# Kernel tuning notes

Hardware: AMD Instinct MI355X
Metric: run time of the kernel (lower is better)

## Reference

```python
import jax, jax.numpy as jnp
import numpy as np

B, S, E, H, F, V = 4, 2048, 1024, 16, 4096, 32000
D = E // H  # head_dim = 64
LN_EPS = 1e-5


def layer_norm(x, g, b):
    mu = jnp.mean(x, axis=-1, keepdims=True)
    var = jnp.mean(jnp.square(x - mu), axis=-1, keepdims=True)
    return (x - mu) * jax.lax.rsqrt(var + LN_EPS) * g + b


def setup_inputs() -> dict:
    key = jax.random.key(0)
    ks = jax.random.split(key, 12)
    s = 0.02
    return {
        "input_ids": jax.random.randint(ks[0], (B, S), 0, V),
        "attention_mask": jnp.ones((B, S), dtype=jnp.int32),
        "emb_table": jax.random.normal(ks[1], (V, E), jnp.float32) * s,
        "Wq": jax.random.normal(ks[2], (E, E), jnp.float32) * s,
        "bq": jnp.zeros((E,), jnp.float32),
        "Wk": jax.random.normal(ks[3], (E, E), jnp.float32) * s,
        "bk": jnp.zeros((E,), jnp.float32),
        "Wv": jax.random.normal(ks[4], (E, E), jnp.float32) * s,
        "bv": jnp.zeros((E,), jnp.float32),
        "Wo": jax.random.normal(ks[5], (E, E), jnp.float32) * s,
        "bo": jnp.zeros((E,), jnp.float32),
        "ln_g": jnp.ones((E,), jnp.float32),
        "ln_b": jnp.zeros((E,), jnp.float32),
        "W1": jax.random.normal(ks[6], (E, F), jnp.float32) * s,
        "b1": jnp.zeros((F,), jnp.float32),
        "W2": jax.random.normal(ks[7], (F, E), jnp.float32) * s,
        "b2": jnp.zeros((E,), jnp.float32),
        "Wp": jax.random.normal(ks[8], (E, 3), jnp.float32) * s,
        "bp": jnp.zeros((3,), jnp.float32),
    }


def reference(input_ids, attention_mask, emb_table, Wq, bq, Wk, bk, Wv, bv,
              Wo, bo, ln_g, ln_b, W1, b1, W2, b2, Wp, bp):
    b, s = input_ids.shape
    x = emb_table[input_ids]                                  # [B,S,E]
    q = (x @ Wq + bq).reshape(b, s, H, D).transpose(0, 2, 1, 3)  # [B,H,S,D]
    k = (x @ Wk + bk).reshape(b, s, H, D).transpose(0, 2, 1, 3)
    v = (x @ Wv + bv).reshape(b, s, H, D).transpose(0, 2, 1, 3)
    scores = jnp.einsum('bhqd,bhkd->bhqk', q, k) / jnp.sqrt(jnp.float32(D))
    mask = attention_mask[:, None, None, :]                   # [B,1,1,S]
    scores = jnp.where(mask == 0, -jnp.inf, scores)
    attn = jax.nn.softmax(scores, axis=-1)
    ctx = jnp.einsum('bhqk,bhkd->bhqd', attn, v)              # [B,H,S,D]
    ctx = ctx.transpose(0, 2, 1, 3).reshape(b, s, E)
    ctx = ctx @ Wo + bo
    h = layer_norm(ctx + x, ln_g, ln_b)
    ff = jax.nn.gelu(h @ W1 + b1, approximate=False) @ W2 + b2
    logits = ff @ Wp + bp                                     # [B,S,3]
    return logits.mean(axis=1)                                # [B,3]
```

## Files before the change

### kernel.cpp

```cpp
#include <hip/hip_runtime.h>
#include <hip/hip_bf16.h>
#include <math.h>

#define BB 4
#define SS 2048
#define EE 1024
#define HH 16
#define DD 64
#define FF 4096

typedef unsigned short u16;
typedef unsigned int u32;
typedef __bf16 bf16x8 __attribute__((ext_vector_type(8)));
typedef float f32x4 __attribute__((ext_vector_type(4)));

static __device__ __forceinline__ float gelu_exact(float v){
  return 0.5f * v * (1.0f + erff(v * 0.70710678118654752f));
}

static __device__ __forceinline__ u16 f2bf(float f){
  union { float f; u32 u; } x; x.f = f;
  u32 r = x.u + 0x7FFFu + ((x.u >> 16) & 1u);
  return (u16)(r >> 16);
}
static __device__ __forceinline__ u16 f2bf_hw(float f){
  union { __bf16 b; u16 u; } c; c.b = (__bf16)f; return c.u;
}
static __device__ __forceinline__ void unpack2(u32 u, float& lo, float& hi){
  union { u32 u; float f; } a, b;
  a.u = u << 16; b.u = u & 0xFFFF0000u;
  lo = a.f; hi = b.f;
}

#define GLOAD_LDS16(g, l) \
  __builtin_amdgcn_global_load_lds((const __attribute__((address_space(1))) void*)(g), \
      (__attribute__((address_space(3))) void*)(l), 16, 0, 0)

__global__ __launch_bounds__(256) void embed_kernel(const int* __restrict__ ids,
    const float* __restrict__ emb, float* __restrict__ xf, u16* __restrict__ xbf){
  int row = blockIdx.x;
  int id  = ids[row];
  float4 v = ((const float4*)(emb + (size_t)id * EE))[threadIdx.x];
  ((float4*)(xf + (size_t)row * EE))[threadIdx.x] = v;
  ushort4 u; u.x = f2bf(v.x); u.y = f2bf(v.y); u.z = f2bf(v.z); u.w = f2bf(v.w);
  ((ushort4*)(xbf + (size_t)row * EE))[threadIdx.x] = u;
}

__global__ __launch_bounds__(256) void prep_weights(const float* __restrict__ Wq,
    const float* __restrict__ Wk, const float* __restrict__ Wv,
    const float* __restrict__ Wo, const float* __restrict__ W1, u16* __restrict__ WT){
  __shared__ float tile[32][33];
  int bid = blockIdx.x;
  const float* W; u16* dst; int N, n0, k0;
  if (bid < 4096){
    W = W1; dst = WT + (size_t)4 * EE * EE; N = FF;
    n0 = (bid & 127) * 32; k0 = (bid >> 7) * 32;
  } else {
    int idx = bid - 4096;
    int which = idx >> 10, t = idx & 1023;
    W = (which == 0) ? Wq : (which == 1) ? Wk : (which == 2) ? Wv : Wo;
    dst = WT + (size_t)which * EE * EE; N = EE;
    n0 = (t & 31) * 32; k0 = (t >> 5) * 32;
  }
  int tx = threadIdx.x & 31, ty = threadIdx.x >> 5;
  #pragma unroll
  for (int i = 0; i < 4; i++)
    tile[ty + 8*i][tx] = W[(size_t)(k0 + ty + 8*i) * N + n0 + tx];
  __syncthreads();
  #pragma unroll
  for (int i = 0; i < 4; i++)
    dst[(size_t)(n0 + ty + 8*i) * EE + k0 + tx] = f2bf(tile[tx][ty + 8*i]);
}

template<int MODE>
__global__ __launch_bounds__(256) void gemm_mfma(const u16* __restrict__ A,
    const u16* __restrict__ WT, const float* __restrict__ bias,
    const float* __restrict__ biasB, const float* __restrict__ biasC,
    u16* __restrict__ C, float* __restrict__ gsum, int M, int N, int K){
  __shared__ __attribute__((aligned(16))) u16 As[128 * 32];
  __shared__ __attribute__((aligned(16))) u16 Bs[128 * 32];

  const int tid = threadIdx.x;
  const int l = tid & 63, w = tid >> 6;
  const int lm = l & 15, lq = l >> 4;
  const int wm = (w >> 1) * 64, wn = (w & 1) * 64;
  const int r0 = blockIdx.y * 128, c0 = blockIdx.x * 128;

  const int srow0 = w * 32 + (l >> 2);
  const int scol  = (l & 3) * 8;
  const u16* Ab = A  + (size_t)(r0 + srow0) * K + scol;
  const u16* Bb = WT + (size_t)(c0 + srow0) * K + scol;
  u16* AsBase0 = &As[(w * 2)     * 512];
  u16* AsBase1 = &As[(w * 2 + 1) * 512];
  u16* BsBase0 = &Bs[(w * 2)     * 512];
  u16* BsBase1 = &Bs[(w * 2 + 1) * 512];

  f32x4 acc[4][4];
  const f32x4 zero = {0.f, 0.f, 0.f, 0.f};
  #pragma unroll
  for (int mi = 0; mi < 4; mi++)
    #pragma unroll
    for (int ni = 0; ni < 4; ni++) acc[mi][ni] = zero;

  for (int k0 = 0; k0 < K; k0 += 32){
    GLOAD_LDS16(Ab + k0,                    AsBase0);
    GLOAD_LDS16(Ab + (size_t)16 * K + k0,   AsBase1);
    GLOAD_LDS16(Bb + k0,                    BsBase0);
    GLOAD_LDS16(Bb + (size_t)16 * K + k0,   BsBase1);
    __syncthreads();

    bf16x8 af[4], bf[4];
    #pragma unroll
    for (int mi = 0; mi < 4; mi++)
      af[mi] = *(const bf16x8*)&As[(wm + mi*16 + lm) * 32 + lq * 8];
    #pragma unroll
    for (int ni = 0; ni < 4; ni++)
      bf[ni] = *(const bf16x8*)&Bs[(wn + ni*16 + lm) * 32 + lq * 8];
    #pragma unroll
    for (int mi = 0; mi < 4; mi++)
      #pragma unroll
      for (int ni = 0; ni < 4; ni++)
        acc[mi][ni] = __builtin_amdgcn_mfma_f32_16x16x32_bf16(af[mi], bf[ni], acc[mi][ni], 0, 0, 0);
    __syncthreads();
  }

  if constexpr (MODE == 0){
    #pragma unroll
    for (int ni = 0; ni < 4; ni++){
      int col = c0 + wn + ni*16 + lm;
      float bcol = bias[col];
      #pragma unroll
      for (int mi = 0; mi < 4; mi++){
        #pragma unroll
        for (int r = 0; r < 4; r++){
          int row = r0 + wm + mi*16 + lq*4 + r;
          C[(size_t)row * N + col] = f2bf(acc[mi][ni][r] + bcol);
        }
      }
    }
  } else if constexpr (MODE == 2){
    #pragma unroll
    for (int ni = 0; ni < 4; ni++){
      int col3 = c0 + wn + ni*16 + lm;
      int sel  = col3 >> 10;
      int colm = col3 & 1023;
      const float* bp_ = (sel == 0) ? bias : ((sel == 1) ? biasB : biasC);
      float bcol = bp_[colm];
      u16* dst = C + (size_t)sel * ((size_t)M * N);
      #pragma unroll
      for (int mi = 0; mi < 4; mi++){
        #pragma unroll
        for (int r = 0; r < 4; r++){
          int row = r0 + wm + mi*16 + lq*4 + r;
          dst[(size_t)row * N + colm] = f2bf(acc[mi][ni][r] + bcol);
        }
      }
    }
  } else {
    const int batch = r0 >> 11;
    #pragma unroll
    for (int ni = 0; ni < 4; ni++){
      int col = c0 + wn + ni*16 + lm;
      float bcol = bias[col];
      float cs = 0.f;
      #pragma unroll
      for (int mi = 0; mi < 4; mi++)
        #pragma unroll
        for (int r = 0; r < 4; r++)
          cs += gelu_exact(acc[mi][ni][r] + bcol);
      cs += __shfl_xor(cs, 16, 64);
      cs += __shfl_xor(cs, 32, 64);
      if (lq == 0) atomicAdd(&gsum[(size_t)batch * N + col], cs);
    }
  }
}

__global__ __launch_bounds__(256, 4) void attn_mfma(const u16* __restrict__ q,
    const u16* __restrict__ k, const u16* __restrict__ v,
    const int* __restrict__ mask, u16* __restrict__ ctx){
  const int bh = blockIdx.y, b = bh >> 4, h = bh & 15;
  const int q0 = blockIdx.x * 128;
  const int tid = threadIdx.x;
  const int w = tid >> 6, l = tid & 63, lm = l & 15, lq = l >> 4;

  __shared__ __attribute__((aligned(16))) u16 smem[128 * 72];
  __shared__ __attribute__((aligned(16))) float mb[64];
  u16* Kt = smem;
  u16* Vt = smem + 64 * 72;

  bf16x8 aq[2][2];
  #pragma unroll
  for (int mg = 0; mg < 2; mg++){
    const u16* qrow = q + (size_t)(b*SS + q0 + w*32 + mg*16 + lm) * EE + h*DD + lq*8;
    aq[mg][0] = *(const bf16x8*)qrow;
    aq[mg][1] = *(const bf16x8*)(qrow + 32);
  }

  f32x4 occ[2][4];
  const f32x4 zero = {0.f,0.f,0.f,0.f};
  #pragma unroll
  for (int mg = 0; mg < 2; mg++)
    #pragma unroll
    for (int mi = 0; mi < 4; mi++) occ[mg][mi] = zero;
  float l_part[2] = {0.f, 0.f};

  const int kkey = tid >> 2, kc16 = (tid & 3) * 16;
  const u16* kbase = k + (size_t)(b*SS + kkey) * EE + h*DD + kc16;
  const int kp = tid & 31, vd0 = (tid >> 5) * 8;
  const u16* vbase0 = v + (size_t)(b*SS + 2*kp) * EE + h*DD + vd0;
  const u16* vbase1 = vbase0 + EE;

  uint4 kr0 = *(const uint4*)(kbase);
  uint4 kr1 = *(const uint4*)(kbase + 8);
  uint4 vr0 = *(const uint4*)(vbase0);
  uint4 vr1 = *(const uint4*)(vbase1);
  float mreg = 0.f;
  if (tid < 64) mreg = (mask[b*SS + tid] != 0) ? 0.f : -1e30f;

  const float SCALE_LOG2E = 0.125f * 1.4426950408889634f;

  for (int t0 = 0; t0 < SS; t0 += 64){
    *(uint4*)&Kt[kkey*72 + kc16]     = kr0;
    *(uint4*)&Kt[kkey*72 + kc16 + 8] = kr1;
    {
      union { uint4 u; u16 s[8]; } va, vb;
      va.u = vr0; vb.u = vr1;
      #pragma unroll
      for (int i = 0; i < 8; i++){
        u32 pk = (u32)va.s[i] | ((u32)vb.s[i] << 16);
        *(u32*)&Vt[(vd0 + i)*72 + 2*kp] = pk;
      }
    }
    if (tid < 64) mb[tid] = mreg;
    __syncthreads();

    if (t0 + 64 < SS){
      kr0 = *(const uint4*)(kbase + (size_t)(t0 + 64) * EE);
      kr1 = *(const uint4*)(kbase + (size_t)(t0 + 64) * EE + 8);
      vr0 = *(const uint4*)(vbase0 + (size_t)(t0 + 64) * EE);
      vr1 = *(const uint4*)(vbase1 + (size_t)(t0 + 64) * EE);
      if (tid < 64) mreg = (mask[b*SS + t0 + 64 + tid] != 0) ? 0.f : -1e30f;
    }

    bf16x8 pb[2][2];
    #pragma unroll
    for (int mg = 0; mg < 2; mg++){
      float lp = 0.f;
      #pragma unroll
      for (int h2 = 0; h2 < 2; h2++){
        u32 pk[2][2];
        #pragma unroll
        for (int np = 0; np < 2; np++){
          int ni = h2*2 + np;
          bf16x8 kf0 = *(const bf16x8*)&Kt[(ni*16 + lm)*72 + lq*8];
          bf16x8 kf1 = *(const bf16x8*)&Kt[(ni*16 + lm)*72 + 32 + lq*8];
          f32x4 sc = zero;
          sc = __builtin_amdgcn_mfma_f32_16x16x32_bf16(kf0, aq[mg][0], sc, 0, 0, 0);
          sc = __builtin_amdgcn_mfma_f32_16x16x32_bf16(kf1, aq[mg][1], sc, 0, 0, 0);
          f32x4 mbv = *(const f32x4*)&mb[ni*16 + lq*4];
          float p[4];
          #pragma unroll
          for (int r = 0; r < 4; r++){
            float s = fminf(fmaf(sc[r], SCALE_LOG2E, mbv[r]), 80.f);
            p[r] = __builtin_amdgcn_exp2f(s);
            lp += p[r];
          }
          pk[np][0] = (u32)f2bf_hw(p[0]) | ((u32)f2bf_hw(p[1]) << 16);
          pk[np][1] = (u32)f2bf_hw(p[2]) | ((u32)f2bf_hw(p[3]) << 16);
        }
        int srcA = lm + 16*((2*lq)     & 3);
        int srcB = lm + 16*((2*lq + 1) & 3);
        u32 x0 = (u32)__shfl((int)pk[0][0], srcA, 64);
        u32 x1 = (u32)__shfl((int)pk[0][1], srcA, 64);
        u32 x2 = (u32)__shfl((int)pk[0][0], srcB, 64);
        u32 x3 = (u32)__shfl((int)pk[0][1], srcB, 64);
        u32 y0 = (u32)__shfl((int)pk[1][0], srcA, 64);
        u32 y1 = (u32)__shfl((int)pk[1][1], srcA, 64);
        u32 y2 = (u32)__shfl((int)pk[1][0], srcB, 64);
        u32 y3 = (u32)__shfl((int)pk[1][1], srcB, 64);
        bool lo = (lq < 2);
        union { u32 u[4]; bf16x8 v; } pu;
        pu.u[0] = lo ? x0 : y0;
        pu.u[1] = lo ? x1 : y1;
        pu.u[2] = lo ? x2 : y2;
        pu.u[3] = lo ? x3 : y3;
        pb[mg][h2] = pu.v;
      }
      l_part[mg] += lp;
    }

    #pragma unroll
    for (int mi = 0; mi < 4; mi++){
      bf16x8 vb0 = *(const bf16x8*)&Vt[(mi*16 + lm)*72 + lq*8];
      bf16x8 vb1 = *(const bf16x8*)&Vt[(mi*16 + lm)*72 + 32 + lq*8];
      #pragma unroll
      for (int mg = 0; mg < 2; mg++){
        occ[mg][mi] = __builtin_amdgcn_mfma_f32_16x16x32_bf16(vb0, pb[mg][0], occ[mg][mi], 0, 0, 0);
        occ[mg][mi] = __builtin_amdgcn_mfma_f32_16x16x32_bf16(vb1, pb[mg][1], occ[mg][mi], 0, 0, 0);
      }
    }
    __syncthreads();
  }

  #pragma unroll
  for (int mg = 0; mg < 2; mg++){
    float s = l_part[mg];
    s += __shfl_xor(s, 16, 64);
    s += __shfl_xor(s, 32, 64);
    float inv = 1.f / s;
    #pragma unroll
    for (int mi = 0; mi < 4; mi++){
      ushort4 o;
      o.x = f2bf(occ[mg][mi][0] * inv);
      o.y = f2bf(occ[mg][mi][1] * inv);
      o.z = f2bf(occ[mg][mi][2] * inv);
      o.w = f2bf(occ[mg][mi][3] * inv);
      *(ushort4*)&smem[(w*32 + mg*16 + lm)*72 + mi*16 + lq*4] = o;
    }
  }
  __syncthreads();
  {
    const int row = tid >> 1, half = tid & 1;
    u16* dst = ctx + (size_t)(b*SS + q0 + row) * EE + h*DD + half*32;
    const u16* src = &smem[row*72 + half*32];
    #pragma unroll
    for (int jj = 0; jj < 4; jj++)
      *(uint4*)(dst + jj*8) = *(const uint4*)(src + jj*8);
  }
}

__global__ __launch_bounds__(256) void ln_kernel(const u16* __restrict__ c2,
    const float* __restrict__ x, const float* __restrict__ g,
    const float* __restrict__ bta, u16* __restrict__ h){
  int row = blockIdx.x, tid = threadIdx.x;
  uint2 cu = ((const uint2*)(c2 + (size_t)row * EE))[tid];
  float c0,c1,c2f,c3;
  unpack2(cu.x, c0, c1); unpack2(cu.y, c2f, c3);
  float4 xv = ((const float4*)(x + (size_t)row * EE))[tid];
  float4 y = make_float4(c0+xv.x, c1+xv.y, c2f+xv.z, c3+xv.w);
  float s  = y.x + y.y + y.z + y.w;
  float ss = y.x*y.x + y.y*y.y + y.z*y.z + y.w*y.w;
  #pragma unroll
  for (int off=32; off; off>>=1){
    s  += __shfl_xor(s,  off, 64);
    ss += __shfl_xor(ss, off, 64);
  }
  __shared__ float rs[4], rss[4];
  int w = tid >> 6;
  if ((tid & 63) == 0){ rs[w] = s; rss[w] = ss; }
  __syncthreads();
  float tot  = rs[0]+rs[1]+rs[2]+rs[3];
  float tots = rss[0]+rss[1]+rss[2]+rss[3];
  float mu  = tot  * (1.f/EE);
  float var = tots * (1.f/EE) - mu*mu;
  float inv = rsqrtf(var + 1e-5f);
  float4 gv = ((const float4*)g)[tid];
  float4 bv = ((const float4*)bta)[tid];
  ushort4 ou;
  ou.x = f2bf((y.x-mu)*inv*gv.x + bv.x);
  ou.y = f2bf((y.y-mu)*inv*gv.y + bv.y);
  ou.z = f2bf((y.z-mu)*inv*gv.z + bv.z);
  ou.w = f2bf((y.w-mu)*inv*gv.w + bv.w);
  ((ushort4*)(h + (size_t)row * EE))[tid] = ou;
}

__global__ __launch_bounds__(256) void w2wp_kernel(const float* __restrict__ W2,
    const float* __restrict__ Wp, float* __restrict__ W2Wp){
  int f0 = blockIdx.x * 8;
  int tid = threadIdx.x;
  int e0 = tid * 4;
  float wp[4][3];
  #pragma unroll
  for (int t = 0; t < 4; t++)
    #pragma unroll
    for (int j = 0; j < 3; j++) wp[t][j] = Wp[(e0 + t)*3 + j];
  __shared__ float red[3][4];
  for (int i = 0; i < 8; i++){
    int f = f0 + i;
    float4 wv = ((const float4*)(W2 + (size_t)f * EE))[tid];
    float w4[4] = {wv.x, wv.y, wv.z, wv.w};
    float p[3] = {0.f, 0.f, 0.f};
    #pragma unroll
    for (int t = 0; t < 4; t++)
      #pragma unroll
      for (int j = 0; j < 3; j++) p[j] += w4[t] * wp[t][j];
    #pragma unroll
    for (int j = 0; j < 3; j++){
      float sj = p[j];
      #pragma unroll
      for (int off = 32; off; off >>= 1) sj += __shfl_xor(sj, off, 64);
      if ((tid & 63) == 0) red[j][tid >> 6] = sj;
    }
    __syncthreads();
    if (tid < 3) W2Wp[f*3 + tid] = red[tid][0] + red[tid][1] + red[tid][2] + red[tid][3];
    __syncthreads();
  }
}

__global__ __launch_bounds__(256) void out_final(const float* __restrict__ gsum,
    const float* __restrict__ W2Wp, const float* __restrict__ b2,
    const float* __restrict__ Wp, const float* __restrict__ bp, float* __restrict__ out){
  int tid = threadIdx.x;
  float part[4][3];
  #pragma unroll
  for (int b = 0; b < 4; b++)
    #pragma unroll
    for (int j = 0; j < 3; j++) part[b][j] = 0.f;
  for (int f = tid; f < FF; f += 256){
    float w0 = W2Wp[f*3], w1 = W2Wp[f*3+1], w2v = W2Wp[f*3+2];
    #pragma unroll
    for (int b = 0; b < 4; b++){
      float g = gsum[b*FF + f] * (1.f/SS);
      part[b][0] += g * w0; part[b][1] += g * w1; part[b][2] += g * w2v;
    }
  }
  float bb[3] = {0.f, 0.f, 0.f};
  for (int e = tid; e < EE; e += 256){
    float bv = b2[e];
    bb[0] += bv * Wp[e*3]; bb[1] += bv * Wp[e*3+1]; bb[2] += bv * Wp[e*3+2];
  }
  __shared__ float red[15][4];
  int lane = tid & 63, w = tid >> 6;
  #pragma unroll
  for (int b = 0; b < 4; b++)
    #pragma unroll
    for (int j = 0; j < 3; j++){
      float s = part[b][j];
      #pragma unroll
      for (int off = 32; off; off >>= 1) s += __shfl_xor(s, off, 64);
      if (lane == 0) red[b*3 + j][w] = s;
    }
  #pragma unroll
  for (int j = 0; j < 3; j++){
    float s = bb[j];
    #pragma unroll
    for (int off = 32; off; off >>= 1) s += __shfl_xor(s, off, 64);
    if (lane == 0) red[12 + j][w] = s;
  }
  __syncthreads();
  if (tid < 12){
    int j = tid % 3;
    float s  = red[tid][0] + red[tid][1] + red[tid][2] + red[tid][3];
    float bj = red[12+j][0] + red[12+j][1] + red[12+j][2] + red[12+j][3];
    out[tid] = s + bj + bp[j];
  }
}

extern "C" void kernel_launch(void* const* d_in, const int* in_sizes, int n_in,
                              void* d_out, int out_size, void* d_ws, size_t ws_size,
                              hipStream_t stream) {
  const int M = BB * SS;
  const int* ids  = (const int*)d_in[0];
  const int* mask = (const int*)d_in[1];
  const float* emb = (const float*)d_in[2];
  const float* Wq = (const float*)d_in[3];  const float* bq = (const float*)d_in[4];
  const float* Wk = (const float*)d_in[5];  const float* bk = (const float*)d_in[6];
  const float* Wv = (const float*)d_in[7];  const float* bv = (const float*)d_in[8];
  const float* Wo = (const float*)d_in[9];  const float* bo = (const float*)d_in[10];
  const float* lg = (const float*)d_in[11]; const float* lb = (const float*)d_in[12];
  const float* W1 = (const float*)d_in[13]; const float* b1 = (const float*)d_in[14];
  const float* W2 = (const float*)d_in[15]; const float* b2 = (const float*)d_in[16];
  const float* Wp = (const float*)d_in[17]; const float* bp = (const float*)d_in[18];

  char* base = (char*)d_ws;
  const size_t SLOTF = (size_t)M * EE;
  float* xf   = (float*)base;
  u16*  xbf   = (u16*)(base + SLOTF*4);
  u16*  qbf   = (u16*)(base + SLOTF*6);
  u16*  kbf   = (u16*)(base + SLOTF*8);
  u16*  vbf   = (u16*)(base + SLOTF*10);
  u16*  ctxbf = (u16*)(base + SLOTF*12);
  u16*  c2bf  = qbf;
  u16*  hbf   = kbf;
  u16*  WqT   = (u16*)(base + SLOTF*14);
  u16*  W1T   = WqT + (size_t)4*EE*EE;
  float* gsum = (float*)(W1T + (size_t)FF*EE);
  float* w2wp = gsum + BB*FF;

  hipMemsetAsync(gsum, 0, BB*FF*sizeof(float), stream);

  embed_kernel<<<M, 256, 0, stream>>>(ids, emb, xf, xbf);

  prep_weights<<<8192, 256, 0, stream>>>(Wq, Wk, Wv, Wo, W1, WqT);
  w2wp_kernel<<<FF/8, 256, 0, stream>>>(W2, Wp, w2wp);

  gemm_mfma<2><<<dim3(3*EE/128, M/128), 256, 0, stream>>>(
      xbf, WqT, bq, bk, bv, qbf, nullptr, M, EE, EE);

  attn_mfma<<<dim3(SS/128, BB*HH), 256, 0, stream>>>(qbf, kbf, vbf, mask, ctxbf);

  gemm_mfma<0><<<dim3(EE/128, M/128), 256, 0, stream>>>(
      ctxbf, WqT + (size_t)3*EE*EE, bo, nullptr, nullptr, c2bf, nullptr, M, EE, EE);

  ln_kernel<<<M, 256, 0, stream>>>(c2bf, xf, lg, lb, hbf);

  gemm_mfma<1><<<dim3(FF/128, M/128), 256, 0, stream>>>(
      hbf, W1T, b1, nullptr, nullptr, nullptr, gsum, M, FF, EE);

  out_final<<<1, 256, 0, stream>>>(gsum, w2wp, b2, Wp, bp, (float*)d_out);
}
```

Measured before the change: 649.3 us.

## Double-buffer GEMM LDS tiles, remap blocks across XCDs, raise MFMA priority in attention

The GEMM kernel now double-buffers its A/B LDS tiles, issuing the next k-tile's global-to-LDS loads before computing on the current one, and keeps one barrier per iteration instead of two. Both the GEMM and attention kernels remap block IDs so that consecutive logical tiles land on the same XCD (stride-8 interleave), aiming for better L2 reuse. The attention kernel lowers its launch-bounds occupancy hint from 4 to 2 and wraps its MFMA sections in s_setprio raises. The extra buffers double GEMM LDS use, and the attention remap hardcodes a grid of 128 blocks per 8 groups, which assumes the fixed problem shape.

```diff
diff --git a/kernel.cpp b/kernel.cpp
--- a/kernel.cpp
+++ b/kernel.cpp
@@ -77,23 +77,27 @@
     const u16* __restrict__ WT, const float* __restrict__ bias,
     const float* __restrict__ biasB, const float* __restrict__ biasC,
     u16* __restrict__ C, float* __restrict__ gsum, int M, int N, int K){
-  __shared__ __attribute__((aligned(16))) u16 As[128 * 32];
-  __shared__ __attribute__((aligned(16))) u16 Bs[128 * 32];
+  __shared__ __attribute__((aligned(16))) u16 As[2][128 * 32];
+  __shared__ __attribute__((aligned(16))) u16 Bs[2][128 * 32];
 
   const int tid = threadIdx.x;
   const int l = tid & 63, w = tid >> 6;
   const int lm = l & 15, lq = l >> 4;
   const int wm = (w >> 1) * 64, wn = (w & 1) * 64;
-  const int r0 = blockIdx.y * 128, c0 = blockIdx.x * 128;
+
+  const int nwg = gridDim.x * gridDim.y;
+  const int bid = blockIdx.y * gridDim.x + blockIdx.x;
+  const int q8  = nwg >> 3;
+  const int lin = (bid & 7) * q8 + (bid >> 3);
+  const int bx  = lin % gridDim.x;
+  const int by  = lin / gridDim.x;
+  const int r0 = by * 128, c0 = bx * 128;
 
   const int srow0 = w * 32 + (l >> 2);
   const int scol  = (l & 3) * 8;
   const u16* Ab = A  + (size_t)(r0 + srow0) * K + scol;
   const u16* Bb = WT + (size_t)(c0 + srow0) * K + scol;
-  u16* AsBase0 = &As[(w * 2)     * 512];
-  u16* AsBase1 = &As[(w * 2 + 1) * 512];
-  u16* BsBase0 = &Bs[(w * 2)     * 512];
-  u16* BsBase1 = &Bs[(w * 2 + 1) * 512];
+  const int sbase = (w * 2) * 512;
 
   f32x4 acc[4][4];
   const f32x4 zero = {0.f, 0.f, 0.f, 0.f};
@@ -102,26 +106,37 @@
     #pragma unroll
     for (int ni = 0; ni < 4; ni++) acc[mi][ni] = zero;
 
+  GLOAD_LDS16(Ab,                  &As[0][sbase]);
+  GLOAD_LDS16(Ab + (size_t)16 * K, &As[0][sbase + 512]);
+  GLOAD_LDS16(Bb,                  &Bs[0][sbase]);
+  GLOAD_LDS16(Bb + (size_t)16 * K, &Bs[0][sbase + 512]);
+  __syncthreads();
+
+  int p = 0;
   for (int k0 = 0; k0 < K; k0 += 32){
-    GLOAD_LDS16(Ab + k0,                    AsBase0);
-    GLOAD_LDS16(Ab + (size_t)16 * K + k0,   AsBase1);
-    GLOAD_LDS16(Bb + k0,                    BsBase0);
-    GLOAD_LDS16(Bb + (size_t)16 * K + k0,   BsBase1);
+    if (k0 + 32 < K){
+      const int pn = p ^ 1;
+      GLOAD_LDS16(Ab + k0 + 32,                   &As[pn][sbase]);
+      GLOAD_LDS16(Ab + (size_t)16 * K + k0 + 32,  &As[pn][sbase + 512]);
+      GLOAD_LDS16(Bb + k0 + 32,                   &Bs[pn][sbase]);
+      GLOAD_LDS16(Bb + (size_t)16 * K + k0 + 32,  &Bs[pn][sbase + 512]);
+    }
+
+    bf16x8 af[4], bfr[4];
+    #pragma unroll
+    for (int mi = 0; mi < 4; mi++)
+      af[mi] = *(const bf16x8*)&As[p][(wm + mi*16 + lm) * 32 + lq * 8];
+    #pragma unroll
+    for (int ni = 0; ni < 4; ni++)
+      bfr[ni] = *(const bf16x8*)&Bs[p][(wn + ni*16 + lm) * 32 + lq * 8];
+    #pragma unroll
+    for (int mi = 0; mi < 4; mi++)
+      #pragma unroll
+      for (int ni = 0; ni < 4; ni++)
+        acc[mi][ni] = __builtin_amdgcn_mfma_f32_16x16x32_bf16(af[mi], bfr[ni], acc[mi][ni], 0, 0, 0);
+
     __syncthreads();
-
-    bf16x8 af[4], bf[4];
-    #pragma unroll
-    for (int mi = 0; mi < 4; mi++)
-      af[mi] = *(const bf16x8*)&As[(wm + mi*16 + lm) * 32 + lq * 8];
-    #pragma unroll
-    for (int ni = 0; ni < 4; ni++)
-      bf[ni] = *(const bf16x8*)&Bs[(wn + ni*16 + lm) * 32 + lq * 8];
-    #pragma unroll
-    for (int mi = 0; mi < 4; mi++)
-      #pragma unroll
-      for (int ni = 0; ni < 4; ni++)
-        acc[mi][ni] = __builtin_amdgcn_mfma_f32_16x16x32_bf16(af[mi], bf[ni], acc[mi][ni], 0, 0, 0);
-    __syncthreads();
+    p ^= 1;
   }
 
   if constexpr (MODE == 0){
@@ -175,11 +190,14 @@
   }
 }
 
-__global__ __launch_bounds__(256, 4) void attn_mfma(const u16* __restrict__ q,
+__global__ __launch_bounds__(256, 2) void attn_mfma(const u16* __restrict__ q,
     const u16* __restrict__ k, const u16* __restrict__ v,
     const int* __restrict__ mask, u16* __restrict__ ctx){
-  const int bh = blockIdx.y, b = bh >> 4, h = bh & 15;
-  const int q0 = blockIdx.x * 128;
+  const int bid = blockIdx.y * gridDim.x + blockIdx.x;
+  const int lin = (bid & 7) * 128 + (bid >> 3);
+  const int qb  = lin & 15, bh = lin >> 4;
+  const int b = bh >> 4, h = bh & 15;
+  const int q0 = qb * 128;
   const int tid = threadIdx.x;
   const int w = tid >> 6, l = tid & 63, lm = l & 15, lq = l >> 4;
 
@@ -255,8 +273,10 @@
           bf16x8 kf0 = *(const bf16x8*)&Kt[(ni*16 + lm)*72 + lq*8];
           bf16x8 kf1 = *(const bf16x8*)&Kt[(ni*16 + lm)*72 + 32 + lq*8];
           f32x4 sc = zero;
+          __builtin_amdgcn_s_setprio(1);
           sc = __builtin_amdgcn_mfma_f32_16x16x32_bf16(kf0, aq[mg][0], sc, 0, 0, 0);
           sc = __builtin_amdgcn_mfma_f32_16x16x32_bf16(kf1, aq[mg][1], sc, 0, 0, 0);
+          __builtin_amdgcn_s_setprio(0);
           f32x4 mbv = *(const f32x4*)&mb[ni*16 + lq*4];
           float p[4];
           #pragma unroll
@@ -289,6 +309,7 @@
       l_part[mg] += lp;
     }
 
+    __builtin_amdgcn_s_setprio(1);
     #pragma unroll
     for (int mi = 0; mi < 4; mi++){
       bf16x8 vb0 = *(const bf16x8*)&Vt[(mi*16 + lm)*72 + lq*8];
@@ -299,6 +320,7 @@
         occ[mg][mi] = __builtin_amdgcn_mfma_f32_16x16x32_bf16(vb1, pb[mg][1], occ[mg][mi], 0, 0, 0);
       }
     }
+    __builtin_amdgcn_s_setprio(0);
     __syncthreads();
   }
 
```

Result: faster. 613.1 us (-5.6%).
